# Performance work log

Measured on AMD Instinct MI355X. Metric: run time of the kernel, lower is better.

The kernel has to match this reference:

```python
import jax, jax.numpy as jnp
import numpy as np

B, N, F_IN, F_OUT = 16, 2048, 512, 512


def setup_inputs() -> dict:
    key = jax.random.key(0)
    k1, k2, k3 = jax.random.split(key, 3)
    x = jax.random.normal(k1, (B, N, F_IN), dtype=jnp.float32)
    adj = jax.random.uniform(k2, (N, N), dtype=jnp.float32)
    # Kaiming uniform fan_out: bound = sqrt(6 / fan_out)
    bound = np.sqrt(6.0 / F_OUT)
    weight = jax.random.uniform(k3, (F_IN, F_OUT), dtype=jnp.float32,
                                minval=-bound, maxval=bound)
    bias = jnp.zeros((F_OUT,), dtype=jnp.float32)
    return {"x": x, "adj": adj, "weight": weight, "bias": bias}


def reference(x, adj, weight, bias):
    # Symmetric degree normalization: D^{-1/2} A D^{-1/2}
    deg = adj.sum(axis=1)                                   # [N]
    deg_inv_sqrt = jnp.where(deg > 0, jax.lax.rsqrt(deg), 0.0)
    # row/column rescale instead of diag matmuls (same math, O(N^2))
    norm_adj = adj * deg_inv_sqrt[:, None] * deg_inv_sqrt[None, :]
    support = jnp.einsum('bni,io->bno', x, weight)          # [B,N,F_OUT]
    output = jnp.einsum('nm,bmo->bno', norm_adj, support)   # [B,N,F_OUT]
    return output + bias
```

## Files before the change

kernel.cpp:

```cpp
#include <hip/hip_runtime.h>
#include <stdint.h>

typedef __attribute__((ext_vector_type(8))) __bf16 bf16x8;
typedef __attribute__((ext_vector_type(4))) float f32x4;
typedef unsigned short u16;

__device__ __forceinline__ u16 f2bf(float f) {
  unsigned u = __builtin_bit_cast(unsigned, f);
  unsigned r = 0x7FFFu + ((u >> 16) & 1u);
  return (u16)((u + r) >> 16);
}

__device__ __forceinline__ void gload16(const void* g, void* l) {
  __builtin_amdgcn_global_load_lds(
      (__attribute__((address_space(1))) void*)(g),
      (__attribute__((address_space(3))) void*)(l),
      16, 0, 0);
}

__global__ void row_deg_k(const float* __restrict__ adj, float* __restrict__ dis, int N) {
  int row = blockIdx.x;
  const float4* a = (const float4*)(adj + (size_t)row * N);
  float s = 0.f;
  for (int j = threadIdx.x; j < N / 4; j += 256) {
    float4 v = a[j];
    s += v.x + v.y + v.z + v.w;
  }
#pragma unroll
  for (int off = 32; off > 0; off >>= 1) s += __shfl_down(s, off, 64);
  __shared__ float wsum[4];
  if ((threadIdx.x & 63) == 0) wsum[threadIdx.x >> 6] = s;
  __syncthreads();
  if (threadIdx.x == 0) {
    float t = wsum[0] + wsum[1] + wsum[2] + wsum[3];
    dis[row] = (t > 0.f) ? (1.0f / sqrtf(t)) : 0.f;
  }
}

__global__ void conv_bf16_k(const float* __restrict__ in, u16* __restrict__ o, int n4) {
  int i = blockIdx.x * 256 + threadIdx.x;
  if (i >= n4) return;
  float4 v = ((const float4*)in)[i];
  ushort4 u;
  u.x = f2bf(v.x); u.y = f2bf(v.y); u.z = f2bf(v.z); u.w = f2bf(v.w);
  ((ushort4*)o)[i] = u;
}

__global__ void conv_wt_k(const float* __restrict__ w, u16* __restrict__ wt) {
  int idx = blockIdx.x * 256 + threadIdx.x;
  int i = idx >> 9, o = idx & 511;
  wt[o * 512 + i] = f2bf(w[idx]);
}

__global__ void make_nadj_k(const float* __restrict__ adj, const float* __restrict__ dis,
                            u16* __restrict__ o, int N) {
  int idx = blockIdx.x * 256 + threadIdx.x;
  int i = idx >> 9;
  int j4 = (idx & 511) * 4;
  float di = dis[i];
  float4 a = ((const float4*)adj)[idx];
  ushort4 u;
  u.x = f2bf(a.x * di * dis[j4 + 0]);
  u.y = f2bf(a.y * di * dis[j4 + 1]);
  u.z = f2bf(a.z * di * dis[j4 + 2]);
  u.w = f2bf(a.w * di * dis[j4 + 3]);
  ((ushort4*)o)[idx] = u;
}

template <int EPI>
__launch_bounds__(512, 2)
__global__ void gemm256_k(const u16* __restrict__ A, int lda,
                          const u16* __restrict__ Bt, int ldb,
                          void* __restrict__ Cv, int ldc,
                          const float* __restrict__ bias, int K,
                          int nMT, int nNT, size_t zBt, size_t zC) {
  __shared__ __align__(16) u16 lds[65536];

  const int tid = threadIdx.x;
  const int lane = tid & 63;
  const int wid = tid >> 6;
  const int wr = wid >> 2;
  const int wc = wid & 3;

  const int flat = blockIdx.x;
  const int wg = (flat & 7) * ((int)gridDim.x >> 3) + (flat >> 3);
  const int m_t = wg % nMT;
  const int rest = wg / nMT;
  const int n_t = rest % nNT;
  const int b = rest / nNT;
  const int rowBase = m_t * 256;
  const int colBase = n_t * 256;
  const u16* Bb = Bt + (size_t)b * zBt;

  const int lr = tid >> 3;
  const int kkl = (tid & 7) * 8;
  const int kswz = kkl ^ ((lr & 7) << 3);
  const u16* gA = A + (size_t)(rowBase + lr) * lda + kswz;
  const u16* gB = Bb + (size_t)(colBase + lr) * ldb + kswz;
  u16* lA = lds + lr * 64 + kkl;
  u16* lB = lds + 32768 + lr * 64 + kkl;

  const int fr = lane & 15;
  const int rswz = (lane & 7) << 3;
  const int kp0 = ((lane >> 4) * 8) ^ rswz;
  const int kp1 = (32 | ((lane >> 4) * 8)) ^ rswz;
  const u16* fA = lds + (wr * 128 + fr) * 64;
  const u16* fB = lds + 32768 + (wc * 64 + fr) * 64;

  f32x4 acc[8][4] = {};
  bf16x8 a0[4], a1[4], b0[4], b1[4];

  const int NT = K >> 6;
  const int NI = NT >> 1;

#define STAGE_A(d, h, t)                                                             \
  do {                                                                               \
    gload16(gA + (size_t)((h) * 64) * lda + (size_t)(t) * 64,                        \
            lA + (d) * 16384 + ((h) * 64) * 64);                                     \
    gload16(gA + (size_t)((h) * 64 + 128) * lda + (size_t)(t) * 64,                  \
            lA + (d) * 16384 + ((h) * 64 + 128) * 64);                               \
  } while (0)

#define STAGE_B(d, h, t)                                                             \
  do {                                                                               \
    gload16(gB + (size_t)((h) * 128) * ldb + (size_t)(t) * 64,                       \
            lB + (d) * 16384 + ((h) * 128) * 64);                                    \
    gload16(gB + (size_t)((h) * 128 + 64) * ldb + (size_t)(t) * 64,                  \
            lB + (d) * 16384 + ((h) * 128 + 64) * 64);                               \
  } while (0)

#define RD_A8(mh, c)                                                                 \
  _Pragma("unroll") for (int m = 0; m < 4; ++m) {                                    \
    a0[m] = *(const bf16x8*)(fA + (c) * 16384 + (mh) * 4096 + m * 1024 + kp0);       \
    a1[m] = *(const bf16x8*)(fA + (c) * 16384 + (mh) * 4096 + m * 1024 + kp1);       \
  }

#define RD_B4(nlo, c)                                                                \
  _Pragma("unroll") for (int n = 0; n < 2; ++n) {                                    \
    b0[(nlo) + n] = *(const bf16x8*)(fB + (c) * 16384 + ((nlo) + n) * 1024 + kp0);   \
    b1[(nlo) + n] = *(const bf16x8*)(fB + (c) * 16384 + ((nlo) + n) * 1024 + kp1);   \
  }

#define MFMA16(mh, nlo)                                                              \
  __builtin_amdgcn_s_setprio(1);                                                     \
  _Pragma("unroll") for (int m = 0; m < 4; ++m) {                                    \
    _Pragma("unroll") for (int n = 0; n < 2; ++n) {                                  \
      acc[(mh) * 4 + m][(nlo) + n] = __builtin_amdgcn_mfma_f32_16x16x32_bf16(        \
          a0[m], b0[(nlo) + n], acc[(mh) * 4 + m][(nlo) + n], 0, 0, 0);              \
      acc[(mh) * 4 + m][(nlo) + n] = __builtin_amdgcn_mfma_f32_16x16x32_bf16(        \
          a1[m], b1[(nlo) + n], acc[(mh) * 4 + m][(nlo) + n], 0, 0, 0);              \
    }                                                                                \
  }                                                                                  \
  __builtin_amdgcn_s_setprio(0)

#define LGKM0() asm volatile("s_waitcnt lgkmcnt(0)" ::: "memory")
#define LGKM8() asm volatile("s_waitcnt lgkmcnt(8)" ::: "memory")
#define VM6()   asm volatile("s_waitcnt vmcnt(6)" ::: "memory")
#define BAR()   __builtin_amdgcn_s_barrier()

  {
    const int t1 = (NT > 1) ? 1 : 0;
    STAGE_A(0, 0, 0);
    STAGE_B(0, 0, 0);
    STAGE_B(0, 1, 0);
    STAGE_A(0, 1, 0);
    STAGE_A(1, 0, t1);
    STAGE_B(1, 0, t1);
    STAGE_B(1, 1, t1);
    VM6();
    BAR();
  }

  for (int i = 0; i < NI; ++i) {
    const int t1 = 2 * i + 1;
    const int s2 = (2 * i + 2 < NT) ? 2 * i + 2 : NT - 1;
    const int s3 = (2 * i + 3 < NT) ? 2 * i + 3 : NT - 1;

    RD_A8(0, 0);
    RD_B4(0, 0);
    STAGE_A(1, 1, t1);
    LGKM8();
    BAR(); LGKM0();
    MFMA16(0, 0);
    BAR();

    RD_B4(2, 0);
    STAGE_A(0, 0, s2);
    BAR(); LGKM0();
    MFMA16(0, 2);
    BAR();

    RD_A8(1, 0);
    STAGE_B(0, 0, s2);
    BAR(); LGKM0();
    MFMA16(1, 2);
    BAR();

    STAGE_B(0, 1, s2);
    BAR(); LGKM0();
    MFMA16(1, 0);
    VM6();
    BAR();

    RD_A8(0, 1);
    RD_B4(0, 1);
    STAGE_A(0, 1, s2);
    LGKM8();
    BAR(); LGKM0();
    MFMA16(0, 0);
    BAR();

    RD_B4(2, 1);
    STAGE_A(1, 0, s3);
    BAR(); LGKM0();
    MFMA16(0, 2);
    BAR();

    RD_A8(1, 1);
    STAGE_B(1, 0, s3);
    BAR(); LGKM0();
    MFMA16(1, 2);
    BAR();

    STAGE_B(1, 1, s3);
    BAR(); LGKM0();
    MFMA16(1, 0);
    VM6();
    BAR();
  }
  asm volatile("s_waitcnt vmcnt(0)" ::: "memory");

  if (EPI == 0) {
    u16* C = (u16*)Cv;
#pragma unroll
    for (int am = 0; am < 8; ++am) {
      const int r = rowBase + wr * 128 + (am >> 2) * 64 + (am & 3) * 16 + (lane >> 4) * 4;
#pragma unroll
      for (int n = 0; n < 4; ++n) {
        const int cc = colBase + wc * 64 + n * 16 + (lane & 15);
        ushort4 v;
        v.x = f2bf(acc[am][n][0]);
        v.y = f2bf(acc[am][n][1]);
        v.z = f2bf(acc[am][n][2]);
        v.w = f2bf(acc[am][n][3]);
        *reinterpret_cast<ushort4*>(&C[(size_t)cc * ldc + r]) = v;
      }
    }
  } else {
    float* C = (float*)Cv + (size_t)b * zC;
#pragma unroll
    for (int n = 0; n < 4; ++n) {
      const int cc = colBase + wc * 64 + n * 16 + (lane & 15);
      const float bv = bias[cc];
#pragma unroll
      for (int am = 0; am < 8; ++am) {
        const int r = rowBase + wr * 128 + (am >> 2) * 64 + (am & 3) * 16 + (lane >> 4) * 4;
#pragma unroll
        for (int j = 0; j < 4; ++j)
          C[(size_t)(r + j) * ldc + cc] = acc[am][n][j] + bv;
      }
    }
  }
#undef STAGE_A
#undef STAGE_B
#undef RD_A8
#undef RD_B4
#undef MFMA16
#undef LGKM0
#undef LGKM8
#undef VM6
#undef BAR
}

extern "C" void kernel_launch(void* const* d_in, const int* in_sizes, int n_in,
                              void* d_out, int out_size, void* d_ws, size_t ws_size,
                              hipStream_t stream) {
  const int B = 16, N = 2048, FIN = 512, FOUT = 512;
  const float* x    = (const float*)d_in[0];
  const float* adj  = (const float*)d_in[1];
  const float* w    = (const float*)d_in[2];
  const float* bias = (const float*)d_in[3];
  float* out = (float*)d_out;
  char* ws = (char*)d_ws;

  float* dis = (float*)ws;
  u16* wt    = (u16*)(ws + 8192);
  u16* nadj  = (u16*)(ws + 532480);
  u16* xb    = (u16*)(ws + 8921088);
  u16* st    = (u16*)(ws + 42475520);

  row_deg_k<<<N, 256, 0, stream>>>(adj, dis, N);
  conv_bf16_k<<<(B * N * FIN / 4 + 255) / 256, 256, 0, stream>>>(x, xb, B * N * FIN / 4);
  conv_wt_k<<<(FIN * FOUT) / 256, 256, 0, stream>>>(w, wt);
  make_nadj_k<<<(N * N / 4) / 256, 256, 0, stream>>>(adj, dis, nadj, N);

  gemm256_k<0><<<dim3(256), 512, 0, stream>>>(
      xb, FIN, wt, FIN, st, B * N, nullptr, FIN, 128, 2, 0, 0);

  gemm256_k<1><<<dim3(256), 512, 0, stream>>>(
      nadj, N, st, B * N, out, FOUT, bias, N, 8, 2,
      (size_t)N, (size_t)N * FOUT);
}
```

Measured before the change: 124.5 us.

## Fuse fp32-to-bf16 conversion of x into the first GEMM's A loading

The separate kernel that converted x to bf16 is removed. A new first-GEMM kernel now reads fp32 x straight from global memory into registers, converts it with the hardware bf16 conversion, and writes it swizzled into LDS in a double-buffered loop, while the weight tile is still staged by direct global-to-LDS loads. This removes one full pass over x (a 64MB read plus a 32MB write) and one launch. In exchange the GEMM reads twice as many A bytes, and its simpler pipeline, with register prefetch and one barrier per K-step, may hide latency less well than the original hand-scheduled kernel.

After: 116.7 us. 6.2% less time.

```diff
diff --git a/kernel.cpp b/kernel.cpp
--- a/kernel.cpp
+++ b/kernel.cpp
@@ -1,4 +1,5 @@
 #include <hip/hip_runtime.h>
+#include <hip/hip_bf16.h>
 #include <stdint.h>
 
 typedef __attribute__((ext_vector_type(8))) __bf16 bf16x8;
@@ -9,6 +10,11 @@
   unsigned u = __builtin_bit_cast(unsigned, f);
   unsigned r = 0x7FFFu + ((u >> 16) & 1u);
   return (u16)((u + r) >> 16);
+}
+
+__device__ __forceinline__ u16 f2bf_hw(float f) {
+  __hip_bfloat16 h = __float2bfloat16(f);
+  return __builtin_bit_cast(u16, h);
 }
 
 __device__ __forceinline__ void gload16(const void* g, void* l) {
@@ -35,15 +41,6 @@
     float t = wsum[0] + wsum[1] + wsum[2] + wsum[3];
     dis[row] = (t > 0.f) ? (1.0f / sqrtf(t)) : 0.f;
   }
-}
-
-__global__ void conv_bf16_k(const float* __restrict__ in, u16* __restrict__ o, int n4) {
-  int i = blockIdx.x * 256 + threadIdx.x;
-  if (i >= n4) return;
-  float4 v = ((const float4*)in)[i];
-  ushort4 u;
-  u.x = f2bf(v.x); u.y = f2bf(v.y); u.z = f2bf(v.z); u.w = f2bf(v.w);
-  ((ushort4*)o)[i] = u;
 }
 
 __global__ void conv_wt_k(const float* __restrict__ w, u16* __restrict__ wt) {
@@ -67,13 +64,133 @@
   ((ushort4*)o)[idx] = u;
 }
 
-template <int EPI>
 __launch_bounds__(512, 2)
-__global__ void gemm256_k(const u16* __restrict__ A, int lda,
-                          const u16* __restrict__ Bt, int ldb,
-                          void* __restrict__ Cv, int ldc,
-                          const float* __restrict__ bias, int K,
-                          int nMT, int nNT, size_t zBt, size_t zC) {
+__global__ void gemm1_xw_k(const float* __restrict__ X,
+                           const u16* __restrict__ Wt,
+                           u16* __restrict__ Ct, int M) {
+  __shared__ __align__(16) u16 lds[65536];
+
+  const int tid = threadIdx.x;
+  const int lane = tid & 63;
+  const int wid = tid >> 6;
+  const int wr = wid >> 2;
+  const int wc = wid & 3;
+
+  const int flat = blockIdx.x;
+  const int wg = (flat & 7) * 32 + (flat >> 3);
+  const int m_t = wg & 127;
+  const int n_t = wg >> 7;
+  const int rowBase = m_t * 256;
+  const int colBase = n_t * 256;
+
+  const int lr = tid >> 3;
+  const int kkl = (tid & 7) * 8;
+  const int s = (lr & 7) << 3;
+  const int kswz = kkl ^ s;
+  const float* gX = X + (size_t)(rowBase + lr) * 512 + kkl;
+  const u16* gB = Wt + (size_t)(colBase + lr) * 512 + kswz;
+  u16* lAsw = lds + lr * 64 + kswz;
+  u16* lB = lds + 32768 + lr * 64 + kkl;
+
+  const int fr = lane & 15;
+  const int rswz = (lane & 7) << 3;
+  const int kp0 = ((lane >> 4) * 8) ^ rswz;
+  const int kp1 = (32 | ((lane >> 4) * 8)) ^ rswz;
+  const u16* fA = lds + (wr * 128 + fr) * 64;
+  const u16* fB = lds + 32768 + (wc * 64 + fr) * 64;
+
+  f32x4 acc[8][4] = {};
+  f32x4 xv[4][2];
+
+  const int NT = 8;
+
+#define LOADX(t)                                                                     \
+  _Pragma("unroll") for (int r4 = 0; r4 < 4; ++r4) {                                 \
+    xv[r4][0] = *(const f32x4*)(gX + (size_t)(r4 * 64) * 512 + (t) * 64);            \
+    xv[r4][1] = *(const f32x4*)(gX + (size_t)(r4 * 64) * 512 + (t) * 64 + 4);        \
+  }
+
+#define STAGE_B1(d, t)                                                               \
+  _Pragma("unroll") for (int r4 = 0; r4 < 4; ++r4)                                   \
+    gload16(gB + (size_t)(r4 * 64) * 512 + (size_t)(t) * 64,                         \
+            lB + (d) * 16384 + r4 * 4096);
+
+#define WRITE_A(d)                                                                   \
+  _Pragma("unroll") for (int r4 = 0; r4 < 4; ++r4) {                                 \
+    bf16x8 v;                                                                        \
+    _Pragma("unroll") for (int i = 0; i < 4; ++i) {                                  \
+      v[i] = __builtin_bit_cast(__bf16, f2bf_hw(xv[r4][0][i]));                      \
+      v[4 + i] = __builtin_bit_cast(__bf16, f2bf_hw(xv[r4][1][i]));                  \
+    }                                                                                \
+    *(bf16x8*)(lAsw + (d) * 16384 + r4 * 4096) = v;                                  \
+  }
+
+  LOADX(0);
+  STAGE_B1(0, 0);
+  WRITE_A(0);
+  __syncthreads();
+
+  for (int t = 0; t < NT; ++t) {
+    const int c = t & 1;
+    const int cn = c ^ 1;
+    const int tn = (t + 1 < NT) ? t + 1 : NT - 1;
+
+    LOADX(tn);
+    STAGE_B1(cn, tn);
+    __builtin_amdgcn_sched_barrier(0);
+
+    bf16x8 a0[8], a1[8], b0[4], b1[4];
+#pragma unroll
+    for (int m = 0; m < 8; ++m) {
+      a0[m] = *(const bf16x8*)(fA + c * 16384 + m * 1024 + kp0);
+      a1[m] = *(const bf16x8*)(fA + c * 16384 + m * 1024 + kp1);
+    }
+#pragma unroll
+    for (int n = 0; n < 4; ++n) {
+      b0[n] = *(const bf16x8*)(fB + c * 16384 + n * 1024 + kp0);
+      b1[n] = *(const bf16x8*)(fB + c * 16384 + n * 1024 + kp1);
+    }
+#pragma unroll
+    for (int m = 0; m < 8; ++m)
+#pragma unroll
+      for (int n = 0; n < 4; ++n)
+        acc[m][n] = __builtin_amdgcn_mfma_f32_16x16x32_bf16(a0[m], b0[n], acc[m][n], 0, 0, 0);
+#pragma unroll
+    for (int m = 0; m < 8; ++m)
+#pragma unroll
+      for (int n = 0; n < 4; ++n)
+        acc[m][n] = __builtin_amdgcn_mfma_f32_16x16x32_bf16(a1[m], b1[n], acc[m][n], 0, 0, 0);
+
+    __builtin_amdgcn_sched_barrier(0);
+    WRITE_A(cn);
+    __syncthreads();
+  }
+
+#pragma unroll
+  for (int m = 0; m < 8; ++m) {
+    const int r = rowBase + wr * 128 + m * 16 + (lane >> 4) * 4;
+#pragma unroll
+    for (int n = 0; n < 4; ++n) {
+      const int cc = colBase + wc * 64 + n * 16 + (lane & 15);
+      ushort4 v;
+      v.x = f2bf(acc[m][n][0]);
+      v.y = f2bf(acc[m][n][1]);
+      v.z = f2bf(acc[m][n][2]);
+      v.w = f2bf(acc[m][n][3]);
+      *reinterpret_cast<ushort4*>(&Ct[(size_t)cc * M + r]) = v;
+    }
+  }
+#undef LOADX
+#undef STAGE_B1
+#undef WRITE_A
+}
+
+__launch_bounds__(512, 2)
+__global__ void gemm2_k(const u16* __restrict__ A, int lda,
+                        const u16* __restrict__ Bt, int ldb,
+                        float* __restrict__ C, int ldc,
+                        const float* __restrict__ bias, int K,
+                        int nMT, int nNT, size_t zBt, size_t zC) {
   __shared__ __align__(16) u16 lds[65536];
 
   const int tid = threadIdx.x;
@@ -230,35 +347,16 @@
   }
   asm volatile("s_waitcnt vmcnt(0)" ::: "memory");
 
-  if (EPI == 0) {
-    u16* C = (u16*)Cv;
+#pragma unroll
+  for (int n = 0; n < 4; ++n) {
+    const int cc = colBase + wc * 64 + n * 16 + (lane & 15);
+    const float bv = bias[cc];
 #pragma unroll
     for (int am = 0; am < 8; ++am) {
       const int r = rowBase + wr * 128 + (am >> 2) * 64 + (am & 3) * 16 + (lane >> 4) * 4;
 #pragma unroll
-      for (int n = 0; n < 4; ++n) {
-        const int cc = colBase + wc * 64 + n * 16 + (lane & 15);
-        ushort4 v;
-        v.x = f2bf(acc[am][n][0]);
-        v.y = f2bf(acc[am][n][1]);
-        v.z = f2bf(acc[am][n][2]);
-        v.w = f2bf(acc[am][n][3]);
-        *reinterpret_cast<ushort4*>(&C[(size_t)cc * ldc + r]) = v;
-      }
-    }
-  } else {
-    float* C = (float*)Cv + (size_t)b * zC;
-#pragma unroll
-    for (int n = 0; n < 4; ++n) {
-      const int cc = colBase + wc * 64 + n * 16 + (lane & 15);
-      const float bv = bias[cc];
-#pragma unroll
-      for (int am = 0; am < 8; ++am) {
-        const int r = rowBase + wr * 128 + (am >> 2) * 64 + (am & 3) * 16 + (lane >> 4) * 4;
-#pragma unroll
-        for (int j = 0; j < 4; ++j)
-          C[(size_t)(r + j) * ldc + cc] = acc[am][n][j] + bv;
-      }
+      for (int j = 0; j < 4; ++j)
+        C[(size_t)b * zC + (size_t)(r + j) * ldc + cc] = acc[am][n][j] + bv;
     }
   }
 #undef STAGE_A
@@ -286,18 +384,15 @@
   float* dis = (float*)ws;
   u16* wt    = (u16*)(ws + 8192);
   u16* nadj  = (u16*)(ws + 532480);
-  u16* xb    = (u16*)(ws + 8921088);
-  u16* st    = (u16*)(ws + 42475520);
+  u16* st    = (u16*)(ws + 8921088);
 
   row_deg_k<<<N, 256, 0, stream>>>(adj, dis, N);
-  conv_bf16_k<<<(B * N * FIN / 4 + 255) / 256, 256, 0, stream>>>(x, xb, B * N * FIN / 4);
   conv_wt_k<<<(FIN * FOUT) / 256, 256, 0, stream>>>(w, wt);
   make_nadj_k<<<(N * N / 4) / 256, 256, 0, stream>>>(adj, dis, nadj, N);
 
-  gemm256_k<0><<<dim3(256), 512, 0, stream>>>(
-      xb, FIN, wt, FIN, st, B * N, nullptr, FIN, 128, 2, 0, 0);
-
-  gemm256_k<1><<<dim3(256), 512, 0, stream>>>(
+  gemm1_xw_k<<<dim3(256), 512, 0, stream>>>(x, wt, st, B * N);
+
+  gemm2_k<<<dim3(256), 512, 0, stream>>>(
       nadj, N, st, B * N, out, FOUT, bias, N, 8, 2,
       (size_t)N, (size_t)N * FOUT);
 }
```
